# Kernel tuning notes

Measured on AMD Instinct MI355X. Metric: run time of the kernel, lower is better.

Reference implementation:

```python
import jax, jax.numpy as jnp
from jax import lax
import numpy as np

B = 4096   # batch
D = 128    # input features
T = 45     # time steps (chosen so Decoder index-length == encoder MAX_len)
H = 512    # encoder_num_hidden == decoder_num_hidden
S = 4      # int((T-1)/9) downsampling branches; encoder LSTM input = 32*S


def setup_inputs() -> dict:
    key = jax.random.key(0)
    ks = jax.random.split(key, 24)
    n = lambda i, shape, s=0.05: jax.random.normal(ks[i], shape, jnp.float32) * s
    return {
        'x': jax.random.normal(ks[0], (B, T, D), jnp.float32),
        'y': jax.random.normal(ks[1], (B, T), jnp.float32),
        # S stacked RCNN branches (identical shapes, independent weights)
        'rcnn_w1': n(2, (S, 16, D)),      'rcnn_b1': n(3, (S, 16)),
        'rcnn_w2': n(4, (S, 32, 16, 3)),  'rcnn_b2': n(5, (S, 32)),
        'rcnn_w3': n(6, (S, 32, 32, 3)),  'rcnn_b3': n(7, (S, 32)),
        # encoder LSTM (input 32*S -> H), torch gate order i,f,g,o
        'enc_wih': n(8, (4 * H, 32 * S)), 'enc_whh': n(9, (4 * H, H)),
        'enc_bih': n(10, (4 * H,)),       'enc_bhh': n(11, (4 * H,)),
        # decoder LSTM (input H+1 -> H)
        'dec_wih': n(12, (4 * H, H + 1)), 'dec_whh': n(13, (4 * H, H)),
        'dec_bih': n(14, (4 * H,)),       'dec_bhh': n(15, (4 * H,)),
        # self-attention over the batch of decoder states
        'wq': n(16, (H, H)), 'wk': n(17, (H, H)), 'wv': n(18, (H, H)),
        'ln_w': n(19, (1, H)), 'ln_b': n(20, (1,)),
    }


def _conv1d(h, w):
    # h: [B, Cin, L], w: [Cout, Cin, 3] -> [B, Cout, L-2] (VALID)
    return lax.conv_general_dilated(h, w, (1,), 'VALID',
                                    dimension_numbers=('NCW', 'OIW', 'NCW'))


def _maxpool2(h):
    # MaxPool kernel (2,1), stride 2 along length (floor semantics)
    b, c, L = h.shape
    L2 = L // 2
    return h[:, :, :L2 * 2].reshape(b, c, L2, 2).max(-1)


def _lstm(xs, wih, whh, bih, bhh):
    # xs: [T, B, I]; returns all hidden states [T, B, H]
    Hh = whh.shape[1]
    bias = bih + bhh
    def step(carry, x_t):
        h, c = carry
        g = x_t @ wih.T + h @ whh.T + bias
        i, f, gg, o = jnp.split(g, 4, axis=-1)
        c = jax.nn.sigmoid(f) * c + jax.nn.sigmoid(i) * jnp.tanh(gg)
        h = jax.nn.sigmoid(o) * jnp.tanh(c)
        return (h, c), h
    z = jnp.zeros((xs.shape[1], Hh), xs.dtype)
    _, hs = lax.scan(step, (z, z), xs)
    return hs


def _forward(x, y, rcnn_w1, rcnn_b1, rcnn_w2, rcnn_b2, rcnn_w3, rcnn_b3,
             enc_wih, enc_whh, enc_bih, enc_bhh,
             dec_wih, dec_whh, dec_bih, dec_bhh, wq, wk, wv, ln_w, ln_b):
    # ---- CNN_downsampling ----
    pieces, maxlen = [], None
    for s in range(1, S + 1):
        xs = x[:, ::s, :]                                  # [B, ceil(T/s), D]
        h = jnp.einsum('bld,cd->bcl', xs, rcnn_w1[s - 1]) + rcnn_b1[s - 1][None, :, None]
        h = _conv1d(h, rcnn_w2[s - 1]) + rcnn_b2[s - 1][None, :, None]
        h = _maxpool2(h)
        h = _conv1d(h, rcnn_w3[s - 1]) + rcnn_b3[s - 1][None, :, None]
        h = _maxpool2(h)
        h = jnp.transpose(h, (0, 2, 1))                    # [B, len_s, 32]
        if s == 1:
            maxlen = h.shape[1]
        else:
            h = jnp.pad(h, ((0, 0), (maxlen - h.shape[1], 0), (0, 0)))
        pieces.append(h)
    feat = jnp.concatenate(pieces, axis=2)                  # [B, T', 32*S]

    # ---- Encoder LSTM (per-step loop in torch == scan here) ----
    hs = _lstm(jnp.transpose(feat, (1, 0, 2)), enc_wih, enc_whh, enc_bih, enc_bhh)
    X_encoded = jnp.transpose(hs, (1, 0, 2))               # [B, T', H]

    # ---- Decoder ----
    Tp = X_encoded.shape[1]
    stp = T // Tp
    idx = np.array(list(range(T - 1, 0, -stp))[::-1])      # static indices
    y_sel = y[:, idx]                                      # [B, T']
    Xd = jnp.concatenate([X_encoded, y_sel[:, :, None]], axis=2)
    hd = _lstm(jnp.transpose(Xd, (1, 0, 2)), dec_wih, dec_whh, dec_bih, dec_bhh)[-1]  # [B, H]

    # ---- SelfAttention over the batch dimension ----
    q, k, v = hd @ wq.T, hd @ wk.T, hd @ wv.T              # [B, H]
    z = (q @ k.T) / jnp.sqrt(jnp.asarray(H, q.dtype))      # [B, B]
    beta = jax.nn.softmax(z, axis=1)
    st = beta @ v                                          # [B, H]
    return jax.nn.sigmoid((st @ ln_w.T + ln_b)[:, 0])      # [B]


def reference(x, y, rcnn_w1, rcnn_b1, rcnn_w2, rcnn_b2, rcnn_w3, rcnn_b3,
              enc_wih, enc_whh, enc_bih, enc_bhh,
              dec_wih, dec_whh, dec_bih, dec_bhh, wq, wk, wv, ln_w, ln_b):
    return _forward(x, y, rcnn_w1, rcnn_b1, rcnn_w2, rcnn_b2, rcnn_w3, rcnn_b3,
                    enc_wih, enc_whh, enc_bih, enc_bhh,
                    dec_wih, dec_whh, dec_bih, dec_bhh, wq, wk, wv, ln_w, ln_b)
```

## Files before the change

kernel.cpp:

```cpp
#include <hip/hip_runtime.h>
#include <cmath>

constexpr int cB  = 4096;
constexpr int cT  = 45;
constexpr int cD  = 128;
constexpr int cH  = 512;
constexpr int cG  = 2048;
constexpr int cTp = 9;
constexpr int cKE = 640;
constexpr int cKD = 1024;

typedef __attribute__((ext_vector_type(8))) short short8;
typedef __attribute__((ext_vector_type(4))) float f32x4;

__device__ __forceinline__ short f2b(float f) {
  unsigned int u = __float_as_uint(f);
  u += 0x7fff + ((u >> 16) & 1);
  return (short)(u >> 16);
}
__device__ __forceinline__ float b2f(short s) {
  return __uint_as_float(((unsigned int)(unsigned short)s) << 16);
}

constexpr long ofFeatB = 0;
constexpr long ofWencB = ofFeatB + (long)cB * cTp * 128 / 2;
constexpr long ofBenc  = ofWencB + (long)cG * cKE / 2;
constexpr long ofWdecB = ofBenc  + cG;
constexpr long ofBdec  = ofWdecB + (long)cG * cKD / 2;
constexpr long ofWy    = ofBdec  + cG;
constexpr long ofGt    = ofWy    + cG;
constexpr long ofCenc  = ofGt    + (long)cB * cG;
constexpr long ofHencB = ofCenc  + (long)cB * cH;
constexpr long ofXencB = ofHencB + (long)cB * cH / 2;
constexpr long ofCdec  = ofXencB + (long)cB * cTp * cH / 2;
constexpr long ofHdecB = ofCdec  + (long)cB * cH;
constexpr long ofWqB   = ofHdecB + (long)cB * cH / 2;
constexpr long ofWkB   = ofWqB   + (long)cH * cH / 2;
constexpr long ofWvB   = ofWkB   + (long)cH * cH / 2;
constexpr long ofQB    = ofWvB   + (long)cH * cH / 2;
constexpr long ofKB    = ofQB    + (long)cB * cH / 2;
constexpr long ofVB    = ofKB    + (long)cB * cH / 2;
constexpr long ofZB    = ofVB    + (long)cB * cH / 2;
constexpr long ofVT    = ofZB    + (long)cB * cB / 2;
constexpr long ofSt    = ofVT    + (long)cH * cB / 2;
constexpr long wsFloats = ofSt   + (long)cB * cH;

__global__ __launch_bounds__(256) void rcnn_kernel(
    const float* __restrict__ x,
    const float* __restrict__ w1, const float* __restrict__ b1,
    const float* __restrict__ w2, const float* __restrict__ b2,
    const float* __restrict__ w3, const float* __restrict__ b3,
    short* __restrict__ featB) {
  const int b = blockIdx.x;
  const int s = blockIdx.y;
  const int stride = s + 1;
  const int L  = (cT + stride - 1) / stride;
  const int L2 = L - 2;
  const int Lp = L2 / 2;
  const int L3 = Lp - 2;
  const int Lf = L3 / 2;
  const int pad = cTp - Lf;
  const int tid = threadIdx.x;

  __shared__ float smem[11180];
  float* xs  = smem;
  float* w1s = smem + 5940;
  float* w2r = smem + 7988;
  float* h1t = smem + 9524;
  float* p2t = smem + 10424;
  float* w3r = smem;
  float* h3t = smem + 3072;
  float* h2t = smem + 5940;

  for (int i = tid; i < L * 128; i += 256) {
    int l = i >> 7, d = i & 127;
    xs[l * 132 + d] = x[((long)b * cT + (long)l * stride) * cD + d];
  }
  for (int i = tid; i < 16 * 128; i += 256) w1s[i] = w1[s * 2048 + i];
  for (int i = tid; i < 32 * 48; i += 256) {
    int c = i / 48, r = i % 48, ci = r / 3, kk = r % 3;
    w2r[(c * 3 + kk) * 16 + ci] = w2[s * 1536 + i];
  }
  __syncthreads();

  for (int i = tid; i < 16 * L; i += 256) {
    int c = i / L, l = i % L;
    const float4* xr = (const float4*)&xs[l * 132];
    const float4* wr = (const float4*)&w1s[c * 128];
    float acc = b1[s * 16 + c];
#pragma unroll
    for (int d4 = 0; d4 < 32; ++d4) {
      float4 xv = xr[d4], wv = wr[d4];
      acc += xv.x * wv.x + xv.y * wv.y + xv.z * wv.z + xv.w * wv.w;
    }
    h1t[l * 20 + c] = acc;
  }
  __syncthreads();

  for (int i = tid; i < 32 * 96; i += 256) {
    int c = i / 96, r = i % 96, ci = r / 3, kk = r % 3;
    w3r[(c * 3 + kk) * 32 + ci] = w3[s * 3072 + i];
  }
  for (int i = tid; i < 32 * L2; i += 256) {
    int c = i / L2, l = i % L2;
    float acc = b2[s * 32 + c];
#pragma unroll
    for (int kk = 0; kk < 3; ++kk) {
      const float4* hp = (const float4*)&h1t[(l + kk) * 20];
      const float4* wp = (const float4*)&w2r[(c * 3 + kk) * 16];
#pragma unroll
      for (int g = 0; g < 4; ++g) {
        float4 hv = hp[g], wv = wp[g];
        acc += hv.x * wv.x + hv.y * wv.y + hv.z * wv.z + hv.w * wv.w;
      }
    }
    h2t[l * 36 + c] = acc;
  }
  __syncthreads();

  for (int i = tid; i < 32 * Lp; i += 256) {
    int l = i >> 5, c = i & 31;
    p2t[l * 36 + c] = fmaxf(h2t[(2 * l) * 36 + c], h2t[(2 * l + 1) * 36 + c]);
  }
  __syncthreads();

  for (int i = tid; i < 32 * L3; i += 256) {
    int c = i / L3, l = i % L3;
    float acc = b3[s * 32 + c];
#pragma unroll
    for (int kk = 0; kk < 3; ++kk) {
      const float4* pp = (const float4*)&p2t[(l + kk) * 36];
      const float4* wp = (const float4*)&w3r[(c * 3 + kk) * 32];
#pragma unroll
      for (int g = 0; g < 8; ++g) {
        float4 pv = pp[g], wv = wp[g];
        acc += pv.x * wv.x + pv.y * wv.y + pv.z * wv.z + pv.w * wv.w;
      }
    }
    h3t[l * 36 + c] = acc;
  }
  __syncthreads();

  for (int i = tid; i < 32 * cTp; i += 256) {
    int c = i / cTp, t = i % cTp;
    float v = 0.0f;
    if (t >= pad) {
      int l = t - pad;
      v = fmaxf(h3t[(2 * l) * 36 + c], h3t[(2 * l + 1) * 36 + c]);
    }
    featB[((long)b * cTp + t) * 128 + s * 32 + c] = f2b(v);
  }
}

__global__ void prep_enc_w(const float* __restrict__ wih, const float* __restrict__ whh,
                           const float* __restrict__ bih, const float* __restrict__ bhh,
                           short* __restrict__ W, float* __restrict__ bias) {
  long i = (long)blockIdx.x * 256 + threadIdx.x;
  if (i < (long)cG * cKE) {
    int g = (int)(i / cKE), k = (int)(i % cKE);
    float v = (k < 128) ? wih[(long)g * 128 + k] : whh[(long)g * 512 + (k - 128)];
    W[i] = f2b(v);
  }
  if (i < cG) bias[i] = bih[i] + bhh[i];
}

__global__ void prep_dec_w(const float* __restrict__ wih, const float* __restrict__ whh,
                           const float* __restrict__ bih, const float* __restrict__ bhh,
                           short* __restrict__ W, float* __restrict__ bias,
                           float* __restrict__ wy) {
  long i = (long)blockIdx.x * 256 + threadIdx.x;
  if (i < (long)cG * cKD) {
    int g = (int)(i / cKD), k = (int)(i % cKD);
    float v = (k < 512) ? wih[(long)g * 513 + k] : whh[(long)g * 512 + (k - 512)];
    W[i] = f2b(v);
  }
  if (i < cG) {
    bias[i] = bih[i] + bhh[i];
    wy[i] = wih[i * 513 + 512];
  }
}

__global__ void conv_f2b(const float* __restrict__ s, short* __restrict__ d, long n) {
  long i = (long)blockIdx.x * 256 + threadIdx.x;
  if (i < n) d[i] = f2b(s[i]);
}

__global__ __launch_bounds__(256) void gemm_bf16_nt(
    const short* __restrict__ A1, int lda1, int K1,
    const short* __restrict__ A2, int lda2,
    const short* __restrict__ W, int ldw,
    const float* __restrict__ bias,
    float* __restrict__ C,
    short* __restrict__ Cb,
    int ldc, int K, float alpha) {
  __shared__ short lsA[128 * 32];
  __shared__ short lsB[128 * 32];
  const int tid  = threadIdx.x;
  const int lane = tid & 63;
  const int wave = tid >> 6;
  const int wr = wave >> 1, wc = wave & 1;
  const long m0 = (long)blockIdx.x * 128;
  const long n0 = (long)blockIdx.y * 128;

  f32x4 acc[4][4];
#pragma unroll
  for (int i = 0; i < 4; ++i)
#pragma unroll
    for (int j = 0; j < 4; ++j) acc[i][j] = (f32x4)0.0f;

  const int segrow = lane >> 2;
  const int chunk  = (lane & 3) * 8;
  const int rbase  = lane & 15;
  const int kk     = (lane >> 4) * 8;

  for (int k0 = 0; k0 < K; k0 += 32) {
    const short* Ab; long alda; int acol;
    if (k0 < K1) { Ab = A1; alda = lda1; acol = k0; }
    else         { Ab = A2; alda = lda2; acol = k0 - K1; }
    __syncthreads();
#pragma unroll
    for (int cs = 0; cs < 2; ++cs) {
      int r = wave * 32 + cs * 16 + segrow;
      const short* ga = Ab + (m0 + r) * alda + acol + chunk;
      __builtin_amdgcn_global_load_lds(
          (const __attribute__((address_space(1))) void*)ga,
          (__attribute__((address_space(3))) void*)&lsA[(wave * 32 + cs * 16) * 32],
          16, 0, 0);
      const short* gw = W + (n0 + r) * (long)ldw + k0 + chunk;
      __builtin_amdgcn_global_load_lds(
          (const __attribute__((address_space(1))) void*)gw,
          (__attribute__((address_space(3))) void*)&lsB[(wave * 32 + cs * 16) * 32],
          16, 0, 0);
    }
    __syncthreads();

    short8 af[4], bf4[4];
#pragma unroll
    for (int i = 0; i < 4; ++i)
      af[i] = *(const short8*)&lsA[(wr * 64 + i * 16 + rbase) * 32 + kk];
#pragma unroll
    for (int j = 0; j < 4; ++j)
      bf4[j] = *(const short8*)&lsB[(wc * 64 + j * 16 + rbase) * 32 + kk];
#pragma unroll
    for (int i = 0; i < 4; ++i)
#pragma unroll
      for (int j = 0; j < 4; ++j)
        acc[i][j] = __builtin_amdgcn_mfma_f32_16x16x32_bf16(af[i], bf4[j], acc[i][j], 0, 0, 0);
  }

#pragma unroll
  for (int i = 0; i < 4; ++i) {
#pragma unroll
    for (int j = 0; j < 4; ++j) {
      long ncol = n0 + wc * 64 + j * 16 + (lane & 15);
      float bv = bias ? bias[ncol] : 0.0f;
#pragma unroll
      for (int r = 0; r < 4; ++r) {
        long mrow = m0 + wr * 64 + i * 16 + (lane >> 4) * 4 + r;
        float v = acc[i][j][r] * alpha + bv;
        if (C)  C[mrow * ldc + ncol] = v;
        if (Cb) Cb[mrow * ldc + ncol] = f2b(v);
      }
    }
  }
}

__global__ __launch_bounds__(256) void lstm_update(
    const float* __restrict__ Gt, float* __restrict__ c, short* __restrict__ hB,
    short* __restrict__ xB, int t,
    const float* __restrict__ y, int yidx, const float* __restrict__ wy) {
  long i = (long)blockIdx.x * 256 + threadIdx.x;
  if (i >= (long)cB * cH) return;
  int b = (int)(i >> 9), j = (int)(i & 511);
  const float* g = Gt + (long)b * cG;
  float ig = g[j], fg = g[cH + j], gg = g[2 * cH + j], og = g[3 * cH + j];
  if (y) {
    float yb = y[(long)b * cT + yidx];
    ig += yb * wy[j];
    fg += yb * wy[cH + j];
    gg += yb * wy[2 * cH + j];
    og += yb * wy[3 * cH + j];
  }
  float si = 1.0f / (1.0f + expf(-ig));
  float sf = 1.0f / (1.0f + expf(-fg));
  float so = 1.0f / (1.0f + expf(-og));
  float cc = sf * c[i] + si * tanhf(gg);
  float hh = so * tanhf(cc);
  c[i] = cc;
  short hb = f2b(hh);
  hB[i] = hb;
  if (xB) xB[((long)b * cTp + t) * cH + j] = hb;
}

__global__ __launch_bounds__(256) void softmax_b(short* __restrict__ zb) {
  const int row = blockIdx.x;
  short* zr = zb + (long)row * cB;
  const int tid = threadIdx.x;
  __shared__ float red[4];

  float e[16];
  float mx = -1e30f;
#pragma unroll
  for (int idx = 0; idx < 16; ++idx) {
    float v = b2f(zr[tid + idx * 256]);
    e[idx] = v;
    mx = fmaxf(mx, v);
  }
  for (int off = 32; off; off >>= 1) mx = fmaxf(mx, __shfl_xor(mx, off));
  if ((tid & 63) == 0) red[tid >> 6] = mx;
  __syncthreads();
  mx = fmaxf(fmaxf(red[0], red[1]), fmaxf(red[2], red[3]));
  __syncthreads();

  float sum = 0.0f;
#pragma unroll
  for (int idx = 0; idx < 16; ++idx) {
    float ev = expf(e[idx] - mx);
    e[idx] = ev;
    sum += ev;
  }
  for (int off = 32; off; off >>= 1) sum += __shfl_xor(sum, off);
  if ((tid & 63) == 0) red[tid >> 6] = sum;
  __syncthreads();
  sum = red[0] + red[1] + red[2] + red[3];
  float inv = 1.0f / sum;
#pragma unroll
  for (int idx = 0; idx < 16; ++idx) zr[tid + idx * 256] = f2b(e[idx] * inv);
}

__global__ __launch_bounds__(256) void transpose_v16(const short* __restrict__ v,
                                                     short* __restrict__ vT) {
  __shared__ short tile[32][33];
  const int bx = blockIdx.x;
  const int by = blockIdx.y;
  const int tx = threadIdx.x & 31, ty = threadIdx.x >> 5;
#pragma unroll
  for (int i = 0; i < 4; ++i)
    tile[ty + i * 8][tx] = v[(long)(bx * 32 + ty + i * 8) * cH + by * 32 + tx];
  __syncthreads();
#pragma unroll
  for (int i = 0; i < 4; ++i)
    vT[(long)(by * 32 + ty + i * 8) * cB + bx * 32 + tx] = tile[tx][ty + i * 8];
}

__global__ __launch_bounds__(256) void final_kernel(const float* __restrict__ st,
                                                    const float* __restrict__ lnw,
                                                    const float* __restrict__ lnb,
                                                    float* __restrict__ out) {
  const int wave = threadIdx.x >> 6, lane = threadIdx.x & 63;
  const int b = blockIdx.x * 4 + wave;
  const float* sr = st + (long)b * cH;
  float acc = 0.0f;
  for (int j = lane; j < cH; j += 64) acc += sr[j] * lnw[j];
  for (int off = 32; off; off >>= 1) acc += __shfl_down(acc, off);
  if (lane == 0) out[b] = 1.0f / (1.0f + expf(-(acc + lnb[0])));
}

extern "C" void kernel_launch(void* const* d_in, const int* in_sizes, int n_in,
                              void* d_out, int out_size, void* d_ws, size_t ws_size,
                              hipStream_t stream) {
  const float* x       = (const float*)d_in[0];
  const float* y       = (const float*)d_in[1];
  const float* rcnn_w1 = (const float*)d_in[2];
  const float* rcnn_b1 = (const float*)d_in[3];
  const float* rcnn_w2 = (const float*)d_in[4];
  const float* rcnn_b2 = (const float*)d_in[5];
  const float* rcnn_w3 = (const float*)d_in[6];
  const float* rcnn_b3 = (const float*)d_in[7];
  const float* enc_wih = (const float*)d_in[8];
  const float* enc_whh = (const float*)d_in[9];
  const float* enc_bih = (const float*)d_in[10];
  const float* enc_bhh = (const float*)d_in[11];
  const float* dec_wih = (const float*)d_in[12];
  const float* dec_whh = (const float*)d_in[13];
  const float* dec_bih = (const float*)d_in[14];
  const float* dec_bhh = (const float*)d_in[15];
  const float* wq      = (const float*)d_in[16];
  const float* wk      = (const float*)d_in[17];
  const float* wv      = (const float*)d_in[18];
  const float* ln_w    = (const float*)d_in[19];
  const float* ln_b    = (const float*)d_in[20];
  float* out = (float*)d_out;

  if (ws_size < (size_t)wsFloats * sizeof(float)) return;

  float* ws    = (float*)d_ws;
  short* featB = (short*)(ws + ofFeatB);
  short* WencB = (short*)(ws + ofWencB);
  float* benc  = ws + ofBenc;
  short* WdecB = (short*)(ws + ofWdecB);
  float* bdec  = ws + ofBdec;
  float* wy    = ws + ofWy;
  float* Gt    = ws + ofGt;
  float* cenc  = ws + ofCenc;
  short* hencB = (short*)(ws + ofHencB);
  short* xencB = (short*)(ws + ofXencB);
  float* cdec  = ws + ofCdec;
  short* hdecB = (short*)(ws + ofHdecB);
  short* wqB   = (short*)(ws + ofWqB);
  short* wkB   = (short*)(ws + ofWkB);
  short* wvB   = (short*)(ws + ofWvB);
  short* qB    = (short*)(ws + ofQB);
  short* kB    = (short*)(ws + ofKB);
  short* vB    = (short*)(ws + ofVB);
  short* zB    = (short*)(ws + ofZB);
  short* vT    = (short*)(ws + ofVT);
  float* st    = ws + ofSt;

  rcnn_kernel<<<dim3(cB, 4), 256, 0, stream>>>(x, rcnn_w1, rcnn_b1, rcnn_w2, rcnn_b2,
                                               rcnn_w3, rcnn_b3, featB);

  prep_enc_w<<<((long)cG * cKE + 255) / 256, 256, 0, stream>>>(enc_wih, enc_whh, enc_bih,
                                                               enc_bhh, WencB, benc);
  prep_dec_w<<<((long)cG * cKD + 255) / 256, 256, 0, stream>>>(dec_wih, dec_whh, dec_bih,
                                                               dec_bhh, WdecB, bdec, wy);
  conv_f2b<<<((long)cH * cH + 255) / 256, 256, 0, stream>>>(wq, wqB, (long)cH * cH);
  conv_f2b<<<((long)cH * cH + 255) / 256, 256, 0, stream>>>(wk, wkB, (long)cH * cH);
  conv_f2b<<<((long)cH * cH + 255) / 256, 256, 0, stream>>>(wv, wvB, (long)cH * cH);

  hipMemsetAsync(cenc, 0, (size_t)cB * cH * sizeof(float), stream);
  hipMemsetAsync(hencB, 0, (size_t)cB * cH * sizeof(short), stream);
  for (int t = 0; t < cTp; ++t) {
    gemm_bf16_nt<<<dim3(cB / 128, cG / 128), 256, 0, stream>>>(
        featB + t * 128, cTp * 128, 128, hencB, cH,
        WencB, cKE, benc, Gt, nullptr, cG, cKE, 1.0f);
    lstm_update<<<((long)cB * cH + 255) / 256, 256, 0, stream>>>(
        Gt, cenc, hencB, xencB, t, nullptr, 0, nullptr);
  }

  hipMemsetAsync(cdec, 0, (size_t)cB * cH * sizeof(float), stream);
  hipMemsetAsync(hdecB, 0, (size_t)cB * cH * sizeof(short), stream);
  for (int t = 0; t < cTp; ++t) {
    int yidx = 4 + 5 * t;
    gemm_bf16_nt<<<dim3(cB / 128, cG / 128), 256, 0, stream>>>(
        xencB + t * cH, cTp * cH, 512, hdecB, cH,
        WdecB, cKD, bdec, Gt, nullptr, cG, cKD, 1.0f);
    lstm_update<<<((long)cB * cH + 255) / 256, 256, 0, stream>>>(
        Gt, cdec, hdecB, nullptr, 0, y, yidx, wy);
  }

  gemm_bf16_nt<<<dim3(cB / 128, cH / 128), 256, 0, stream>>>(
      hdecB, cH, cH, nullptr, 0, wqB, cH, nullptr, nullptr, qB, cH, cH, 1.0f);
  gemm_bf16_nt<<<dim3(cB / 128, cH / 128), 256, 0, stream>>>(
      hdecB, cH, cH, nullptr, 0, wkB, cH, nullptr, nullptr, kB, cH, cH, 1.0f);
  gemm_bf16_nt<<<dim3(cB / 128, cH / 128), 256, 0, stream>>>(
      hdecB, cH, cH, nullptr, 0, wvB, cH, nullptr, nullptr, vB, cH, cH, 1.0f);

  const float alpha = 1.0f / sqrtf((float)cH);
  gemm_bf16_nt<<<dim3(cB / 128, cB / 128), 256, 0, stream>>>(
      qB, cH, cH, nullptr, 0, kB, cH, nullptr, nullptr, zB, cB, cH, alpha);

  softmax_b<<<cB, 256, 0, stream>>>(zB);

  transpose_v16<<<dim3(cB / 32, cH / 32), 256, 0, stream>>>(vB, vT);
  gemm_bf16_nt<<<dim3(cB / 128, cH / 128), 256, 0, stream>>>(
      zB, cB, cB, nullptr, 0, vT, cB, nullptr, st, nullptr, cH, cB, 1.0f);

  final_kernel<<<cB / 4, 256, 0, stream>>>(st, ln_w, ln_b, out);
}
```

Baseline: 1.474 ms.

## Fuse LSTM cell update into gate GEMM epilogue and merge QKV projections

Interleaves the gate rows of the LSTM weights so that each group of four adjacent output columns holds i,f,g,o for one hidden unit. This lets the gate GEMM apply the cell update in its epilogue through an LDS scratch tile, which removes the 4096x2048 fp32 gate buffer round trip and the separate lstm_update launch. Hidden state is double-buffered because the GEMM now reads h while writing the next h. Q/K/V are computed in one GEMM over concatenated weights, and the RCNN convolutions are register-blocked (2 positions x 4 channels per thread) with padded LDS strides.

```diff
diff --git a/kernel.cpp b/kernel.cpp
--- a/kernel.cpp
+++ b/kernel.cpp
@@ -21,6 +21,9 @@
 __device__ __forceinline__ float b2f(short s) {
   return __uint_as_float(((unsigned int)(unsigned short)s) << 16);
 }
+__device__ __forceinline__ float dot4(float4 a, float4 b) {
+  return a.x * b.x + a.y * b.y + a.z * b.z + a.w * b.w;
+}
 
 constexpr long ofFeatB = 0;
 constexpr long ofWencB = ofFeatB + (long)cB * cTp * 128 / 2;
@@ -28,19 +31,16 @@
 constexpr long ofWdecB = ofBenc  + cG;
 constexpr long ofBdec  = ofWdecB + (long)cG * cKD / 2;
 constexpr long ofWy    = ofBdec  + cG;
-constexpr long ofGt    = ofWy    + cG;
-constexpr long ofCenc  = ofGt    + (long)cB * cG;
-constexpr long ofHencB = ofCenc  + (long)cB * cH;
-constexpr long ofXencB = ofHencB + (long)cB * cH / 2;
+constexpr long ofCenc  = ofWy    + cG;
+constexpr long ofH0enc = ofCenc  + (long)cB * cH;
+constexpr long ofH1enc = ofH0enc + (long)cB * cH / 2;
+constexpr long ofXencB = ofH1enc + (long)cB * cH / 2;
 constexpr long ofCdec  = ofXencB + (long)cB * cTp * cH / 2;
-constexpr long ofHdecB = ofCdec  + (long)cB * cH;
-constexpr long ofWqB   = ofHdecB + (long)cB * cH / 2;
-constexpr long ofWkB   = ofWqB   + (long)cH * cH / 2;
-constexpr long ofWvB   = ofWkB   + (long)cH * cH / 2;
-constexpr long ofQB    = ofWvB   + (long)cH * cH / 2;
-constexpr long ofKB    = ofQB    + (long)cB * cH / 2;
-constexpr long ofVB    = ofKB    + (long)cB * cH / 2;
-constexpr long ofZB    = ofVB    + (long)cB * cH / 2;
+constexpr long ofH0dec = ofCdec  + (long)cB * cH;
+constexpr long ofH1dec = ofH0dec + (long)cB * cH / 2;
+constexpr long ofWqkv  = ofH1dec + (long)cB * cH / 2;
+constexpr long ofQkvB  = ofWqkv  + (long)3 * cH * cH / 2;
+constexpr long ofZB    = ofQkvB  + (long)cB * 3 * cH / 2;
 constexpr long ofVT    = ofZB    + (long)cB * cB / 2;
 constexpr long ofSt    = ofVT    + (long)cH * cB / 2;
 constexpr long wsFloats = ofSt   + (long)cB * cH;
@@ -62,82 +62,142 @@
   const int pad = cTp - Lf;
   const int tid = threadIdx.x;
 
-  __shared__ float smem[11180];
+  __shared__ float smem[11628];
   float* xs  = smem;
   float* w1s = smem + 5940;
-  float* w2r = smem + 7988;
-  float* h1t = smem + 9524;
-  float* p2t = smem + 10424;
+  float* w2r = smem + 8052;
+  float* h1t = smem + 9972;
+  float* p2t = smem + 10872;
   float* w3r = smem;
-  float* h3t = smem + 3072;
+  float* h3t = smem + 3456;
   float* h2t = smem + 5940;
 
   for (int i = tid; i < L * 128; i += 256) {
     int l = i >> 7, d = i & 127;
     xs[l * 132 + d] = x[((long)b * cT + (long)l * stride) * cD + d];
   }
-  for (int i = tid; i < 16 * 128; i += 256) w1s[i] = w1[s * 2048 + i];
+  for (int i = tid; i < 16 * 128; i += 256) {
+    int c = i >> 7, d = i & 127;
+    w1s[c * 132 + d] = w1[s * 2048 + i];
+  }
   for (int i = tid; i < 32 * 48; i += 256) {
     int c = i / 48, r = i % 48, ci = r / 3, kk = r % 3;
-    w2r[(c * 3 + kk) * 16 + ci] = w2[s * 1536 + i];
-  }
-  __syncthreads();
-
-  for (int i = tid; i < 16 * L; i += 256) {
-    int c = i / L, l = i % L;
-    const float4* xr = (const float4*)&xs[l * 132];
-    const float4* wr = (const float4*)&w1s[c * 128];
-    float acc = b1[s * 16 + c];
-#pragma unroll
-    for (int d4 = 0; d4 < 32; ++d4) {
-      float4 xv = xr[d4], wv = wr[d4];
-      acc += xv.x * wv.x + xv.y * wv.y + xv.z * wv.z + xv.w * wv.w;
-    }
-    h1t[l * 20 + c] = acc;
+    w2r[(c * 3 + kk) * 20 + ci] = w2[s * 1536 + i];
+  }
+  __syncthreads();
+
+  {
+    const int c4 = tid & 3, lp = tid >> 2;
+    const int Lh = (L + 1) >> 1;
+    if (lp < Lh) {
+      int l0 = 2 * lp, l1 = l0 + 1;
+      bool has1 = l1 < L;
+      int l1r = has1 ? l1 : l0;
+      float a0[4], a1[4];
+#pragma unroll
+      for (int cc = 0; cc < 4; ++cc) { a0[cc] = b1[s * 16 + 4 * c4 + cc]; a1[cc] = a0[cc]; }
+      const float4* x0 = (const float4*)&xs[l0 * 132];
+      const float4* x1 = (const float4*)&xs[l1r * 132];
+#pragma unroll 8
+      for (int d4 = 0; d4 < 32; ++d4) {
+        float4 xv0 = x0[d4], xv1 = x1[d4];
+#pragma unroll
+        for (int cc = 0; cc < 4; ++cc) {
+          float4 wv = *(const float4*)&w1s[(4 * c4 + cc) * 132 + 4 * d4];
+          a0[cc] += dot4(xv0, wv);
+          a1[cc] += dot4(xv1, wv);
+        }
+      }
+#pragma unroll
+      for (int cc = 0; cc < 4; ++cc) {
+        h1t[l0 * 20 + 4 * c4 + cc] = a0[cc];
+        if (has1) h1t[l1 * 20 + 4 * c4 + cc] = a1[cc];
+      }
+    }
   }
   __syncthreads();
 
   for (int i = tid; i < 32 * 96; i += 256) {
     int c = i / 96, r = i % 96, ci = r / 3, kk = r % 3;
-    w3r[(c * 3 + kk) * 32 + ci] = w3[s * 3072 + i];
-  }
-  for (int i = tid; i < 32 * L2; i += 256) {
-    int c = i / L2, l = i % L2;
-    float acc = b2[s * 32 + c];
-#pragma unroll
-    for (int kk = 0; kk < 3; ++kk) {
-      const float4* hp = (const float4*)&h1t[(l + kk) * 20];
-      const float4* wp = (const float4*)&w2r[(c * 3 + kk) * 16];
-#pragma unroll
-      for (int g = 0; g < 4; ++g) {
-        float4 hv = hp[g], wv = wp[g];
-        acc += hv.x * wv.x + hv.y * wv.y + hv.z * wv.z + hv.w * wv.w;
-      }
-    }
-    h2t[l * 36 + c] = acc;
-  }
-  __syncthreads();
-
-  for (int i = tid; i < 32 * Lp; i += 256) {
-    int l = i >> 5, c = i & 31;
-    p2t[l * 36 + c] = fmaxf(h2t[(2 * l) * 36 + c], h2t[(2 * l + 1) * 36 + c]);
-  }
-  __syncthreads();
-
-  for (int i = tid; i < 32 * L3; i += 256) {
-    int c = i / L3, l = i % L3;
-    float acc = b3[s * 32 + c];
-#pragma unroll
-    for (int kk = 0; kk < 3; ++kk) {
-      const float4* pp = (const float4*)&p2t[(l + kk) * 36];
-      const float4* wp = (const float4*)&w3r[(c * 3 + kk) * 32];
-#pragma unroll
-      for (int g = 0; g < 8; ++g) {
-        float4 pv = pp[g], wv = wp[g];
-        acc += pv.x * wv.x + pv.y * wv.y + pv.z * wv.z + pv.w * wv.w;
-      }
-    }
-    h3t[l * 36 + c] = acc;
+    w3r[(c * 3 + kk) * 36 + ci] = w3[s * 3072 + i];
+  }
+  {
+    const int c8 = tid & 7, lp = tid >> 3;
+    const int L2h = (L2 + 1) >> 1;
+    if (lp < L2h) {
+      int l0 = 2 * lp, l1 = l0 + 1;
+      bool has1 = l1 < L2;
+      float a0[4], a1[4];
+#pragma unroll
+      for (int cc = 0; cc < 4; ++cc) { a0[cc] = b2[s * 32 + 4 * c8 + cc]; a1[cc] = a0[cc]; }
+#pragma unroll
+      for (int kk = 0; kk < 3; ++kk) {
+        float4 hA[4], hB4[4];
+#pragma unroll
+        for (int g = 0; g < 4; ++g) {
+          hA[g] = *(const float4*)&h1t[(l0 + kk) * 20 + 4 * g];
+          hB4[g] = *(const float4*)&h1t[(l0 + kk + 1) * 20 + 4 * g];
+        }
+#pragma unroll
+        for (int cc = 0; cc < 4; ++cc) {
+          const float4* wv = (const float4*)&w2r[((4 * c8 + cc) * 3 + kk) * 20];
+          float s0 = 0, s1 = 0;
+#pragma unroll
+          for (int g = 0; g < 4; ++g) { s0 += dot4(hA[g], wv[g]); s1 += dot4(hB4[g], wv[g]); }
+          a0[cc] += s0; a1[cc] += s1;
+        }
+      }
+#pragma unroll
+      for (int cc = 0; cc < 4; ++cc) {
+        h2t[l0 * 36 + 4 * c8 + cc] = a0[cc];
+        if (has1) h2t[l1 * 36 + 4 * c8 + cc] = a1[cc];
+      }
+    }
+  }
+  __syncthreads();
+
+  for (int i = tid; i < 8 * Lp; i += 256) {
+    int l = i >> 3, g = i & 7;
+    float4 u = *(const float4*)&h2t[(2 * l) * 36 + 4 * g];
+    float4 v = *(const float4*)&h2t[(2 * l + 1) * 36 + 4 * g];
+    float4 m; m.x = fmaxf(u.x, v.x); m.y = fmaxf(u.y, v.y);
+    m.z = fmaxf(u.z, v.z); m.w = fmaxf(u.w, v.w);
+    *(float4*)&p2t[l * 36 + 4 * g] = m;
+  }
+  __syncthreads();
+
+  {
+    const int c8 = tid & 7, lp = tid >> 3;
+    const int L3h = (L3 + 1) >> 1;
+    if (lp < L3h) {
+      int l0 = 2 * lp, l1 = l0 + 1;
+      bool has1 = l1 < L3;
+      float a0[4], a1[4];
+#pragma unroll
+      for (int cc = 0; cc < 4; ++cc) { a0[cc] = b3[s * 32 + 4 * c8 + cc]; a1[cc] = a0[cc]; }
+#pragma unroll
+      for (int kk = 0; kk < 3; ++kk) {
+        float4 pA[8], pB8[8];
+#pragma unroll
+        for (int g = 0; g < 8; ++g) {
+          pA[g] = *(const float4*)&p2t[(l0 + kk) * 36 + 4 * g];
+          pB8[g] = *(const float4*)&p2t[(l0 + kk + 1) * 36 + 4 * g];
+        }
+#pragma unroll
+        for (int cc = 0; cc < 4; ++cc) {
+          const float4* wv = (const float4*)&w3r[((4 * c8 + cc) * 3 + kk) * 36];
+          float s0 = 0, s1 = 0;
+#pragma unroll
+          for (int g = 0; g < 8; ++g) { s0 += dot4(pA[g], wv[g]); s1 += dot4(pB8[g], wv[g]); }
+          a0[cc] += s0; a1[cc] += s1;
+        }
+      }
+#pragma unroll
+      for (int cc = 0; cc < 4; ++cc) {
+        h3t[l0 * 36 + 4 * c8 + cc] = a0[cc];
+        if (has1) h3t[l1 * 36 + 4 * c8 + cc] = a1[cc];
+      }
+    }
   }
   __syncthreads();
 
@@ -157,11 +217,15 @@
                            short* __restrict__ W, float* __restrict__ bias) {
   long i = (long)blockIdx.x * 256 + threadIdx.x;
   if (i < (long)cG * cKE) {
-    int g = (int)(i / cKE), k = (int)(i % cKE);
-    float v = (k < 128) ? wih[(long)g * 128 + k] : whh[(long)g * 512 + (k - 128)];
+    int gp = (int)(i / cKE), k = (int)(i % cKE);
+    int og = (gp & 3) * 512 + (gp >> 2);
+    float v = (k < 128) ? wih[(long)og * 128 + k] : whh[(long)og * 512 + (k - 128)];
     W[i] = f2b(v);
   }
-  if (i < cG) bias[i] = bih[i] + bhh[i];
+  if (i < cG) {
+    int og = ((int)i & 3) * 512 + ((int)i >> 2);
+    bias[i] = bih[og] + bhh[og];
+  }
 }
 
 __global__ void prep_dec_w(const float* __restrict__ wih, const float* __restrict__ whh,
@@ -170,31 +234,42 @@
                            float* __restrict__ wy) {
   long i = (long)blockIdx.x * 256 + threadIdx.x;
   if (i < (long)cG * cKD) {
-    int g = (int)(i / cKD), k = (int)(i % cKD);
-    float v = (k < 512) ? wih[(long)g * 513 + k] : whh[(long)g * 512 + (k - 512)];
+    int gp = (int)(i / cKD), k = (int)(i % cKD);
+    int og = (gp & 3) * 512 + (gp >> 2);
+    float v = (k < 512) ? wih[(long)og * 513 + k] : whh[(long)og * 512 + (k - 512)];
     W[i] = f2b(v);
   }
   if (i < cG) {
-    bias[i] = bih[i] + bhh[i];
-    wy[i] = wih[i * 513 + 512];
-  }
-}
-
-__global__ void conv_f2b(const float* __restrict__ s, short* __restrict__ d, long n) {
+    int og = ((int)i & 3) * 512 + ((int)i >> 2);
+    bias[i] = bih[og] + bhh[og];
+    wy[i] = wih[(long)og * 513 + 512];
+  }
+}
+
+__global__ void prep_qkv_w(const float* __restrict__ wq, const float* __restrict__ wk,
+                           const float* __restrict__ wv, short* __restrict__ W) {
   long i = (long)blockIdx.x * 256 + threadIdx.x;
-  if (i < n) d[i] = f2b(s[i]);
-}
-
+  if (i >= (long)3 * cH * cH) return;
+  int r = (int)(i / cH), k = (int)(i % cH);
+  float v = (r < 512) ? wq[(long)r * cH + k]
+          : (r < 1024) ? wk[(long)(r - 512) * cH + k]
+                       : wv[(long)(r - 1024) * cH + k];
+  W[i] = f2b(v);
+}
+
+template <int MODE>
 __global__ __launch_bounds__(256) void gemm_bf16_nt(
     const short* __restrict__ A1, int lda1, int K1,
     const short* __restrict__ A2, int lda2,
     const short* __restrict__ W, int ldw,
     const float* __restrict__ bias,
-    float* __restrict__ C,
-    short* __restrict__ Cb,
-    int ldc, int K, float alpha) {
+    float* __restrict__ C, short* __restrict__ Cb, int ldc,
+    int K, float alpha,
+    float* __restrict__ cst, short* __restrict__ hB, short* __restrict__ xB, int t,
+    const float* __restrict__ y, int yidx, const float* __restrict__ wy) {
   __shared__ short lsA[128 * 32];
   __shared__ short lsB[128 * 32];
+  __shared__ float scr[4 * 256];
   const int tid  = threadIdx.x;
   const int lane = tid & 63;
   const int wave = tid >> 6;
@@ -248,48 +323,59 @@
         acc[i][j] = __builtin_amdgcn_mfma_f32_16x16x32_bf16(af[i], bf4[j], acc[i][j], 0, 0, 0);
   }
 
-#pragma unroll
-  for (int i = 0; i < 4; ++i) {
-#pragma unroll
-    for (int j = 0; j < 4; ++j) {
-      long ncol = n0 + wc * 64 + j * 16 + (lane & 15);
-      float bv = bias ? bias[ncol] : 0.0f;
-#pragma unroll
-      for (int r = 0; r < 4; ++r) {
-        long mrow = m0 + wr * 64 + i * 16 + (lane >> 4) * 4 + r;
-        float v = acc[i][j][r] * alpha + bv;
-        if (C)  C[mrow * ldc + ncol] = v;
-        if (Cb) Cb[mrow * ldc + ncol] = f2b(v);
-      }
-    }
-  }
-}
-
-__global__ __launch_bounds__(256) void lstm_update(
-    const float* __restrict__ Gt, float* __restrict__ c, short* __restrict__ hB,
-    short* __restrict__ xB, int t,
-    const float* __restrict__ y, int yidx, const float* __restrict__ wy) {
-  long i = (long)blockIdx.x * 256 + threadIdx.x;
-  if (i >= (long)cB * cH) return;
-  int b = (int)(i >> 9), j = (int)(i & 511);
-  const float* g = Gt + (long)b * cG;
-  float ig = g[j], fg = g[cH + j], gg = g[2 * cH + j], og = g[3 * cH + j];
-  if (y) {
-    float yb = y[(long)b * cT + yidx];
-    ig += yb * wy[j];
-    fg += yb * wy[cH + j];
-    gg += yb * wy[2 * cH + j];
-    og += yb * wy[3 * cH + j];
-  }
-  float si = 1.0f / (1.0f + expf(-ig));
-  float sf = 1.0f / (1.0f + expf(-fg));
-  float so = 1.0f / (1.0f + expf(-og));
-  float cc = sf * c[i] + si * tanhf(gg);
-  float hh = so * tanhf(cc);
-  c[i] = cc;
-  short hb = f2b(hh);
-  hB[i] = hb;
-  if (xB) xB[((long)b * cTp + t) * cH + j] = hb;
+  if constexpr (MODE == 0) {
+#pragma unroll
+    for (int i = 0; i < 4; ++i) {
+#pragma unroll
+      for (int j = 0; j < 4; ++j) {
+        long ncol = n0 + wc * 64 + j * 16 + (lane & 15);
+        float bv = bias ? bias[ncol] : 0.0f;
+#pragma unroll
+        for (int r = 0; r < 4; ++r) {
+          long mrow = m0 + wr * 64 + i * 16 + (lane >> 4) * 4 + r;
+          float v = acc[i][j][r] * alpha + bv;
+          if (C)  C[mrow * ldc + ncol] = v;
+          if (Cb) Cb[mrow * ldc + ncol] = f2b(v);
+        }
+      }
+    }
+  } else {
+    float* scrw = scr + wave * 256;
+    const int c0 = lane & 15;
+    const int r0 = (lane >> 4) * 4;
+    const int rrow = lane >> 2;
+    const int jj = lane & 3;
+#pragma unroll
+    for (int i = 0; i < 4; ++i) {
+      long b = m0 + wr * 64 + i * 16 + rrow;
+      float yb = y ? y[b * cT + yidx] : 0.0f;
+#pragma unroll
+      for (int jf = 0; jf < 4; ++jf) {
+#pragma unroll
+        for (int rr = 0; rr < 4; ++rr) scrw[(r0 + rr) * 16 + c0] = acc[i][jf][rr];
+        long nbase = n0 + wc * 64 + jf * 16;
+        long j = (nbase >> 2) + jj;
+        f32x4 g4 = *(f32x4*)&scrw[rrow * 16 + jj * 4];
+        f32x4 b4 = *(const f32x4*)&bias[4 * j];
+        float ig = g4[0] + b4[0], fg = g4[1] + b4[1];
+        float gg = g4[2] + b4[2], og = g4[3] + b4[3];
+        if (y) {
+          f32x4 w4 = *(const f32x4*)&wy[4 * j];
+          ig += yb * w4[0]; fg += yb * w4[1]; gg += yb * w4[2]; og += yb * w4[3];
+        }
+        float si = 1.0f / (1.0f + expf(-ig));
+        float sf = 1.0f / (1.0f + expf(-fg));
+        float so = 1.0f / (1.0f + expf(-og));
+        long idx = b * cH + j;
+        float cc = sf * cst[idx] + si * tanhf(gg);
+        float hh = so * tanhf(cc);
+        cst[idx] = cc;
+        short hb = f2b(hh);
+        hB[idx] = hb;
+        if (xB) xB[(b * cTp + t) * cH + j] = hb;
+      }
+    }
+  }
 }
 
 __global__ __launch_bounds__(256) void softmax_b(short* __restrict__ zb) {
@@ -328,7 +414,7 @@
   for (int idx = 0; idx < 16; ++idx) zr[tid + idx * 256] = f2b(e[idx] * inv);
 }
 
-__global__ __launch_bounds__(256) void transpose_v16(const short* __restrict__ v,
+__global__ __launch_bounds__(256) void transpose_v16(const short* __restrict__ v, int ldv,
                                                      short* __restrict__ vT) {
   __shared__ short tile[32][33];
   const int bx = blockIdx.x;
@@ -336,7 +422,7 @@
   const int tx = threadIdx.x & 31, ty = threadIdx.x >> 5;
 #pragma unroll
   for (int i = 0; i < 4; ++i)
-    tile[ty + i * 8][tx] = v[(long)(bx * 32 + ty + i * 8) * cH + by * 32 + tx];
+    tile[ty + i * 8][tx] = v[(long)(bx * 32 + ty + i * 8) * ldv + by * 32 + tx];
   __syncthreads();
 #pragma unroll
   for (int i = 0; i < 4; ++i)
@@ -390,19 +476,14 @@
   float* benc  = ws + ofBenc;
   short* WdecB = (short*)(ws + ofWdecB);
   float* bdec  = ws + ofBdec;
-  float* wy    = ws + ofWy;
-  float* Gt    = ws + ofGt;
+  float* wyI   = ws + ofWy;
   float* cenc  = ws + ofCenc;
-  short* hencB = (short*)(ws + ofHencB);
+  short* hEnc[2] = { (short*)(ws + ofH0enc), (short*)(ws + ofH1enc) };
   short* xencB = (short*)(ws + ofXencB);
   float* cdec  = ws + ofCdec;
-  short* hdecB = (short*)(ws + ofHdecB);
-  short* wqB   = (short*)(ws + ofWqB);
-  short* wkB   = (short*)(ws + ofWkB);
-  short* wvB   = (short*)(ws + ofWvB);
-  short* qB    = (short*)(ws + ofQB);
-  short* kB    = (short*)(ws + ofKB);
-  short* vB    = (short*)(ws + ofVB);
+  short* hDec[2] = { (short*)(ws + ofH0dec), (short*)(ws + ofH1dec) };
+  short* Wqkv  = (short*)(ws + ofWqkv);
+  short* qkvB  = (short*)(ws + ofQkvB);
   short* zB    = (short*)(ws + ofZB);
   short* vT    = (short*)(ws + ofVT);
   float* st    = ws + ofSt;
@@ -413,48 +494,47 @@
   prep_enc_w<<<((long)cG * cKE + 255) / 256, 256, 0, stream>>>(enc_wih, enc_whh, enc_bih,
                                                                enc_bhh, WencB, benc);
   prep_dec_w<<<((long)cG * cKD + 255) / 256, 256, 0, stream>>>(dec_wih, dec_whh, dec_bih,
-                                                               dec_bhh, WdecB, bdec, wy);
-  conv_f2b<<<((long)cH * cH + 255) / 256, 256, 0, stream>>>(wq, wqB, (long)cH * cH);
-  conv_f2b<<<((long)cH * cH + 255) / 256, 256, 0, stream>>>(wk, wkB, (long)cH * cH);
-  conv_f2b<<<((long)cH * cH + 255) / 256, 256, 0, stream>>>(wv, wvB, (long)cH * cH);
+                                                               dec_bhh, WdecB, bdec, wyI);
+  prep_qkv_w<<<((long)3 * cH * cH + 255) / 256, 256, 0, stream>>>(wq, wk, wv, Wqkv);
 
   hipMemsetAsync(cenc, 0, (size_t)cB * cH * sizeof(float), stream);
-  hipMemsetAsync(hencB, 0, (size_t)cB * cH * sizeof(short), stream);
+  hipMemsetAsync(hEnc[0], 0, (size_t)cB * cH * sizeof(short), stream);
   for (int t = 0; t < cTp; ++t) {
-    gemm_bf16_nt<<<dim3(cB / 128, cG / 128), 256, 0, stream>>>(
-        featB + t * 128, cTp * 128, 128, hencB, cH,
-        WencB, cKE, benc, Gt, nullptr, cG, cKE, 1.0f);
-    lstm_update<<<((long)cB * cH + 255) / 256, 256, 0, stream>>>(
-        Gt, cenc, hencB, xencB, t, nullptr, 0, nullptr);
+    gemm_bf16_nt<1><<<dim3(cB / 128, cG / 128), 256, 0, stream>>>(
+        featB + t * 128, cTp * 128, 128, hEnc[t & 1], cH,
+        WencB, cKE, benc, nullptr, nullptr, 0, cKE, 1.0f,
+        cenc, hEnc[(t + 1) & 1], xencB, t, nullptr, 0, nullptr);
   }
 
   hipMemsetAsync(cdec, 0, (size_t)cB * cH * sizeof(float), stream);
-  hipMemsetAsync(hdecB, 0, (size_t)cB * cH * sizeof(short), stream);
+  hipMemsetAsync(hDec[0], 0, (size_t)cB * cH * sizeof(short), stream);
   for (int t = 0; t < cTp; ++t) {
     int yidx = 4 + 5 * t;
-    gemm_bf16_nt<<<dim3(cB / 128, cG / 128), 256, 0, stream>>>(
-        xencB + t * cH, cTp * cH, 512, hdecB, cH,
-        WdecB, cKD, bdec, Gt, nullptr, cG, cKD, 1.0f);
-    lstm_update<<<((long)cB * cH + 255) / 256, 256, 0, stream>>>(
-        Gt, cdec, hdecB, nullptr, 0, y, yidx, wy);
-  }
-
-  gemm_bf16_nt<<<dim3(cB / 128, cH / 128), 256, 0, stream>>>(
-      hdecB, cH, cH, nullptr, 0, wqB, cH, nullptr, nullptr, qB, cH, cH, 1.0f);
-  gemm_bf16_nt<<<dim3(cB / 128, cH / 128), 256, 0, stream>>>(
-      hdecB, cH, cH, nullptr, 0, wkB, cH, nullptr, nullptr, kB, cH, cH, 1.0f);
-  gemm_bf16_nt<<<dim3(cB / 128, cH / 128), 256, 0, stream>>>(
-      hdecB, cH, cH, nullptr, 0, wvB, cH, nullptr, nullptr, vB, cH, cH, 1.0f);
+    gemm_bf16_nt<1><<<dim3(cB / 128, cG / 128), 256, 0, stream>>>(
+        xencB + t * cH, cTp * cH, 512, hDec[t & 1], cH,
+        WdecB, cKD, bdec, nullptr, nullptr, 0, cKD, 1.0f,
+        cdec, hDec[(t + 1) & 1], nullptr, t, y, yidx, wyI);
+  }
+  short* hd = hDec[cTp & 1];
+
+  gemm_bf16_nt<0><<<dim3(cB / 128, 3 * cH / 128), 256, 0, stream>>>(
+      hd, cH, cH, nullptr, 0, Wqkv, cH, nullptr,
+      nullptr, qkvB, 3 * cH, cH, 1.0f,
+      nullptr, nullptr, nullptr, 0, nullptr, 0, nullptr);
 
   const float alpha = 1.0f / sqrtf((float)cH);
-  gemm_bf16_nt<<<dim3(cB / 128, cB / 128), 256, 0, stream>>>(
-      qB, cH, cH, nullptr, 0, kB, cH, nullptr, nullptr, zB, cB, cH, alpha);
+  gemm_bf16_nt<0><<<dim3(cB / 128, cB / 128), 256, 0, stream>>>(
+      qkvB, 3 * cH, cH, nullptr, 0, qkvB + cH, 3 * cH, nullptr,
+      nullptr, zB, cB, cH, alpha,
+      nullptr, nullptr, nullptr, 0, nullptr, 0, nullptr);
 
   softmax_b<<<cB, 256, 0, stream>>>(zB);
 
-  transpose_v16<<<dim3(cB / 32, cH / 32), 256, 0, stream>>>(vB, vT);
-  gemm_bf16_nt<<<dim3(cB / 128, cH / 128), 256, 0, stream>>>(
-      zB, cB, cB, nullptr, 0, vT, cB, nullptr, st, nullptr, cH, cB, 1.0f);
+  transpose_v16<<<dim3(cB / 32, cH / 32), 256, 0, stream>>>(qkvB + 2 * cH, 3 * cH, vT);
+  gemm_bf16_nt<0><<<dim3(cB / 128, cH / 128), 256, 0, stream>>>(
+      zB, cB, cB, nullptr, 0, vT, cB, nullptr,
+      st, nullptr, cH, cB, 1.0f,
+      nullptr, nullptr, nullptr, 0, nullptr, 0, nullptr);
 
   final_kernel<<<cB / 4, 256, 0, stream>>>(st, ln_w, ln_b, out);
 }
```

Measured after the change: 1.870 ms. 1.27x slower.
